# Performance work log

Measured on AMD Instinct MI355X. Metric: run time of the kernel, lower is better.

The kernel has to match this reference:

```python
import jax, jax.numpy as jnp
import numpy as np

BATCH, IN, HID, OUT = 8192, 784, 4096, 10


def setup_inputs() -> dict:
    key = jax.random.key(0)
    k_x, k_w1, k_b1, k_w2, k_b2 = jax.random.split(key, 5)
    return {
        "x": jax.random.normal(k_x, (BATCH, IN), dtype=jnp.float32),
        "W1": jax.random.normal(k_w1, (HID, IN), dtype=jnp.float32) * 0.05,
        "b1": jax.random.normal(k_b1, (HID,), dtype=jnp.float32) * 0.05,
        "W2": jax.random.normal(k_w2, (OUT, HID), dtype=jnp.float32) * 0.05,
        "b2": jax.random.normal(k_b2, (OUT,), dtype=jnp.float32) * 0.05,
    }


def reference(x, W1, b1, W2, b2):
    # x: [B, 784] -- first layer, so the input is NOT binarized (BNN convention
    # for in_features == 784); only the weight is sign-quantized.
    x = x.reshape(-1, IN)
    Wb1 = jnp.sign(W1)                       # binarized weights in {-1, 0, +1}
    h = jnp.einsum("bi,hi->bh", x, Wb1) + b1  # BinarizeLinear fc1
    h = jnp.clip(h, -1.0, 1.0)               # Hardtanh
    out = jnp.einsum("bh,oh->bo", h, W2) + b2  # plain float fc2
    return out
```

## Files before the change

kernel.cpp:

```cpp
#include <hip/hip_runtime.h>
#include <cstdint>


#define BATCH 8192
#define IN_F  784
#define HID   4096
#define OUT_F 10
#define KP    832
#define NKT   13
#define BM    256
#define BN    256
#define BK    64
#define NCT   (HID / BN)
#define HCS   264

typedef unsigned short u16;
typedef __attribute__((ext_vector_type(4))) unsigned short u16x4;
typedef __attribute__((ext_vector_type(8)))  _Float16 f16x8;
typedef __attribute__((ext_vector_type(4)))  float    f32x4;

#define BARRIER() do { asm volatile("" ::: "memory"); \
                       __builtin_amdgcn_s_barrier();  \
                       asm volatile("" ::: "memory"); } while (0)
#define WAITV(n)  asm volatile("s_waitcnt vmcnt(" #n ")" ::: "memory")
#define LGKM0()   asm volatile("s_waitcnt lgkmcnt(0)" ::: "memory")

__device__ __forceinline__ u16 f2h(float f) {
  union { _Float16 h; u16 u; } c;
  c.h = (_Float16)f;
  return c.u;
}

__device__ __forceinline__ void gl_lds16(const void* g, void* l) {
  __builtin_amdgcn_global_load_lds(
      (const __attribute__((address_space(1))) uint32_t*)g,
      (__attribute__((address_space(3))) uint32_t*)l, 16, 0, 0);
}

__global__ void prep_kernel(const float* __restrict__ x, const float* __restrict__ W1,
                            const float* __restrict__ W2,
                            u16* __restrict__ xh, u16* __restrict__ wh,
                            u16* __restrict__ w2h) {
  const int stride = gridDim.x * blockDim.x;
  const int gid = blockIdx.x * blockDim.x + threadIdx.x;
  const int KP4 = KP / 4;
  const int IN4 = IN_F / 4;
  const float4* x4 = (const float4*)x;
  const float4* w4 = (const float4*)W1;
  for (int i = gid; i < BATCH * KP4; i += stride) {
    int b = i / KP4, k = i - b * KP4;
    u16x4 o = {0, 0, 0, 0};
    if (k < IN4) {
      float4 v = x4[(size_t)b * IN4 + k];
      o[0] = f2h(v.x); o[1] = f2h(v.y); o[2] = f2h(v.z); o[3] = f2h(v.w);
    }
    *(u16x4*)&xh[(size_t)b * KP + k * 4] = o;
  }
  for (int i = gid; i < HID * KP4; i += stride) {
    int h = i / KP4, k = i - h * KP4;
    u16x4 o = {0, 0, 0, 0};
    if (k < IN4) {
      float4 v = w4[(size_t)h * IN4 + k];
      o[0] = v.x > 0.f ? 0x3C00 : (v.x < 0.f ? 0xBC00 : 0);
      o[1] = v.y > 0.f ? 0x3C00 : (v.y < 0.f ? 0xBC00 : 0);
      o[2] = v.z > 0.f ? 0x3C00 : (v.z < 0.f ? 0xBC00 : 0);
      o[3] = v.w > 0.f ? 0x3C00 : (v.w < 0.f ? 0xBC00 : 0);
    }
    *(u16x4*)&wh[(size_t)h * KP + k * 4] = o;
  }
  for (int i = gid; i < 16 * HID; i += stride) {
    int o = i >> 12, k = i & (HID - 1);
    w2h[i] = (o < OUT_F) ? f2h(W2[o * HID + k]) : (u16)0;
  }
}

__global__ void __launch_bounds__(512, 2) gemm_kernel(
    const u16* __restrict__ xh, const u16* __restrict__ wh,
    const u16* __restrict__ w2h, const float* __restrict__ b1,
    float* __restrict__ part) {
  __shared__ union {
    struct { u16 A[2][BM * BK]; u16 B[2][BN * BK]; } m;
    struct { u16 hc[128 * HCS]; u16 w2[16 * 256]; } e;
  } sm;

  const int t   = threadIdx.x;
  const int ct  = blockIdx.x;
  const int br  = blockIdx.y;
  const int w   = t >> 6;
  const int l   = t & 63;
  const int wm  = w >> 2;
  const int wn  = w & 3;
  const int g   = l >> 4;
  const int r16 = l & 15;
  const int swz = (r16 & 7) << 3;

  const int  srow  = t >> 3;
  const int  sslot = (t & 7) ^ (srow & 7);
  const u16* gA = xh + (size_t)(br * BM) * KP + sslot * 8;
  const u16* gB = wh + (size_t)(ct * BN) * KP + sslot * 8;

  auto stA2 = [&](int tile, int h) {
    const int b = tile & 1;
#pragma unroll
    for (int c = 2 * h; c < 2 * h + 2; ++c)
      gl_lds16(gA + (size_t)(c * 64 + srow) * KP + tile * BK,
               &sm.m.A[b][c * 4096 + t * 8]);
  };
  auto stB2 = [&](int tile, int h) {
    const int b = tile & 1;
#pragma unroll
    for (int c = 2 * h; c < 2 * h + 2; ++c)
      gl_lds16(gB + (size_t)(c * 64 + srow) * KP + tile * BK,
               &sm.m.B[b][c * 4096 + t * 8]);
  };
  auto rdA = [&](int p, int MI, int kk) -> f16x8 {
    int row = MI * 32 + wm * 16 + r16;
    return *(const f16x8*)&sm.m.A[p][row * 64 + ((kk * 32 + g * 8) ^ swz)];
  };
  auto rdB = [&](int p, int nj, int kk) -> f16x8 {
    int row = wn * 64 + nj * 16 + r16;
    return *(const f16x8*)&sm.m.B[p][row * 64 + ((kk * 32 + g * 8) ^ swz)];
  };

  f32x4 acc[8][4] = {};
  f16x8 af[4], bf0[4], bf1[4];

#define MFMA16(MH, BF) do {                                           \
    __builtin_amdgcn_s_setprio(1);                                    \
    _Pragma("unroll") for (int mi_ = 0; mi_ < 4; ++mi_)               \
      _Pragma("unroll") for (int nj_ = 0; nj_ < 4; ++nj_)             \
        acc[(MH) * 4 + mi_][nj_] = __builtin_amdgcn_mfma_f32_16x16x32_f16( \
            af[mi_], BF[nj_], acc[(MH) * 4 + mi_][nj_], 0, 0, 0);     \
    __builtin_amdgcn_s_setprio(0);                                    \
  } while (0)

  stA2(0, 0); stB2(0, 0); stB2(0, 1); stA2(0, 1);
  WAITV(2);
  BARRIER();

  for (int tt = 0; tt < NKT; ++tt) {
    const int  p    = tt & 1;
    const bool more = (tt + 1 < NKT);

#pragma unroll
    for (int mi = 0; mi < 4; ++mi) af[mi] = rdA(p, mi, 0);
#pragma unroll
    for (int nj = 0; nj < 4; ++nj) bf0[nj] = rdB(p, nj, 0);
    if (more) stA2(tt + 1, 0);
    BARRIER();
    MFMA16(0, bf0);
    if (more) { WAITV(2); } else { WAITV(0); }
    BARRIER();

#pragma unroll
    for (int mi = 0; mi < 4; ++mi) af[mi] = rdA(p, 4 + mi, 0);
    if (more) stB2(tt + 1, 0);
    BARRIER();
    MFMA16(1, bf0);
    BARRIER();

#pragma unroll
    for (int mi = 0; mi < 4; ++mi) af[mi] = rdA(p, mi, 1);
#pragma unroll
    for (int nj = 0; nj < 4; ++nj) bf1[nj] = rdB(p, nj, 1);
    if (more) stB2(tt + 1, 1);
    BARRIER();
    MFMA16(0, bf1);
    BARRIER();

#pragma unroll
    for (int mi = 0; mi < 4; ++mi) af[mi] = rdA(p, 4 + mi, 1);
    if (more) stA2(tt + 1, 1);
    BARRIER();
    MFMA16(1, bf1);
    if (more) WAITV(2);
    BARRIER();
  }

  LGKM0();
  BARRIER();
  {
    int row = t >> 5, sp = t & 31;
    int ls = (sp & 24) | ((sp ^ row) & 7);
    gl_lds16(w2h + (size_t)row * HID + ct * BN + ls * 8, &sm.e.w2[t * 8]);
  }
  float b1v[4];
#pragma unroll
  for (int ni = 0; ni < 4; ++ni) b1v[ni] = b1[ct * BN + wn * 64 + ni * 16 + r16];

  float* partBase = part + ((size_t)ct * BATCH + br * BM) * 16;

#pragma unroll
  for (int p = 0; p < 2; ++p) {
    if (p == 1) BARRIER();
#pragma unroll
    for (int mi = 0; mi < 4; ++mi)
#pragma unroll
      for (int ni = 0; ni < 4; ++ni)
#pragma unroll
        for (int r = 0; r < 4; ++r) {
          float v = acc[p * 4 + mi][ni][r] + b1v[ni];
          v = fminf(fmaxf(v, -1.f), 1.f);
          sm.e.hc[(mi * 32 + wm * 16 + g * 4 + r) * HCS + wn * 64 + ni * 16 + r16] = f2h(v);
        }
    if (p == 0) { WAITV(0); }
    BARRIER();
    f32x4 acc2 = {};
#pragma unroll
    for (int kk = 0; kk < 8; ++kk) {
      f16x8 a2 = *(const f16x8*)&sm.e.hc[(w * 16 + r16) * HCS + kk * 32 + g * 8];
      int s   = kk * 4 + g;
      int sp2 = (s & 24) | ((s ^ r16) & 7);
      f16x8 b2f = *(const f16x8*)&sm.e.w2[r16 * 256 + sp2 * 8];
      acc2 = __builtin_amdgcn_mfma_f32_16x16x32_f16(a2, b2f, acc2, 0, 0, 0);
    }
#pragma unroll
    for (int r = 0; r < 4; ++r)
      partBase[(size_t)(p * 128 + w * 16 + g * 4 + r) * 16 + r16] = acc2[r];
  }
}

__global__ void reduce_kernel(const float* __restrict__ part, const float* __restrict__ b2,
                              float* __restrict__ out) {
  int i = blockIdx.x * blockDim.x + threadIdx.x;
  if (i >= BATCH * OUT_F) return;
  int b = i / OUT_F, o = i - b * OUT_F;
  float acc = b2[o];
#pragma unroll
  for (int c = 0; c < NCT; ++c)
    acc += part[((size_t)c * BATCH + b) * 16 + o];
  out[i] = acc;
}

extern "C" void kernel_launch(void* const* d_in, const int* in_sizes, int n_in,
                              void* d_out, int out_size, void* d_ws, size_t ws_size,
                              hipStream_t stream) {
  const float* x  = (const float*)d_in[0];
  const float* W1 = (const float*)d_in[1];
  const float* b1 = (const float*)d_in[2];
  const float* W2 = (const float*)d_in[3];
  const float* b2 = (const float*)d_in[4];
  float* out = (float*)d_out;

  u16* xh  = (u16*)d_ws;
  u16* wh  = xh + (size_t)BATCH * KP;
  u16* w2h = wh + (size_t)HID * KP;
  float* part = (float*)(w2h + 16 * HID);

  hipLaunchKernelGGL(prep_kernel, dim3(2048), dim3(256), 0, stream, x, W1, W2, xh, wh, w2h);
  hipLaunchKernelGGL(gemm_kernel, dim3(NCT, BATCH / BM), dim3(512), 0, stream,
                     xh, wh, w2h, b1, part);
  hipLaunchKernelGGL(reduce_kernel, dim3((BATCH * OUT_F + 255) / 256), dim3(256), 0, stream,
                     part, b2, out);
}
```

Measured before the change: 65.77 us.

## Triple-buffer B tiles and prefetch them two K-steps ahead

Grows the weight-tile LDS staging from two to three buffers so B tiles are loaded two iterations ahead, while A stays double-buffered and both of its halves are issued earlier in the iteration. The goal is to hide more global-to-LDS load latency behind the MFMA work and to drop the mid-iteration vmcnt wait. The cost is extra LDS (now about 160KB per block) and a retuned wait-count schedule, which leaves little headroom and could stall if the counts are off.

```diff
diff --git a/kernel.cpp b/kernel.cpp
--- a/kernel.cpp
+++ b/kernel.cpp
@@ -79,7 +79,7 @@
     const u16* __restrict__ w2h, const float* __restrict__ b1,
     float* __restrict__ part) {
   __shared__ union {
-    struct { u16 A[2][BM * BK]; u16 B[2][BN * BK]; } m;
+    struct { u16 A[2][BM * BK]; u16 B[3][BN * BK]; } m;
     struct { u16 hc[128 * HCS]; u16 w2[16 * 256]; } e;
   } sm;
 
@@ -106,20 +106,19 @@
       gl_lds16(gA + (size_t)(c * 64 + srow) * KP + tile * BK,
                &sm.m.A[b][c * 4096 + t * 8]);
   };
-  auto stB2 = [&](int tile, int h) {
-    const int b = tile & 1;
+  auto stB2 = [&](int tile, int h, int s) {
 #pragma unroll
     for (int c = 2 * h; c < 2 * h + 2; ++c)
       gl_lds16(gB + (size_t)(c * 64 + srow) * KP + tile * BK,
-               &sm.m.B[b][c * 4096 + t * 8]);
+               &sm.m.B[s][c * 4096 + t * 8]);
   };
   auto rdA = [&](int p, int MI, int kk) -> f16x8 {
     int row = MI * 32 + wm * 16 + r16;
     return *(const f16x8*)&sm.m.A[p][row * 64 + ((kk * 32 + g * 8) ^ swz)];
   };
-  auto rdB = [&](int p, int nj, int kk) -> f16x8 {
+  auto rdB = [&](int s, int nj, int kk) -> f16x8 {
     int row = wn * 64 + nj * 16 + r16;
-    return *(const f16x8*)&sm.m.B[p][row * 64 + ((kk * 32 + g * 8) ^ swz)];
+    return *(const f16x8*)&sm.m.B[s][row * 64 + ((kk * 32 + g * 8) ^ swz)];
   };
 
   f32x4 acc[8][4] = {};
@@ -134,27 +133,31 @@
     __builtin_amdgcn_s_setprio(0);                                    \
   } while (0)
 
-  stA2(0, 0); stB2(0, 0); stB2(0, 1); stA2(0, 1);
-  WAITV(2);
+  stB2(0, 0, 0); stB2(0, 1, 0);
+  stA2(0, 0);    stA2(0, 1);
+  stB2(1, 0, 1); stB2(1, 1, 1);
+  WAITV(4);
   BARRIER();
 
   for (int tt = 0; tt < NKT; ++tt) {
-    const int  p    = tt & 1;
-    const bool more = (tt + 1 < NKT);
+    const int  p      = tt & 1;
+    const int  bs     = tt - (tt / 3) * 3;
+    const int  bs2    = (bs >= 1) ? bs - 1 : 2;
+    const bool a_more = (tt + 1 < NKT);
+    const bool b_more = (tt + 2 < NKT);
 
 #pragma unroll
     for (int mi = 0; mi < 4; ++mi) af[mi] = rdA(p, mi, 0);
 #pragma unroll
-    for (int nj = 0; nj < 4; ++nj) bf0[nj] = rdB(p, nj, 0);
-    if (more) stA2(tt + 1, 0);
+    for (int nj = 0; nj < 4; ++nj) bf0[nj] = rdB(bs, nj, 0);
+    if (a_more) stA2(tt + 1, 0);
     BARRIER();
     MFMA16(0, bf0);
-    if (more) { WAITV(2); } else { WAITV(0); }
     BARRIER();
 
 #pragma unroll
     for (int mi = 0; mi < 4; ++mi) af[mi] = rdA(p, 4 + mi, 0);
-    if (more) stB2(tt + 1, 0);
+    if (a_more) stA2(tt + 1, 1);
     BARRIER();
     MFMA16(1, bf0);
     BARRIER();
@@ -162,18 +165,19 @@
 #pragma unroll
     for (int mi = 0; mi < 4; ++mi) af[mi] = rdA(p, mi, 1);
 #pragma unroll
-    for (int nj = 0; nj < 4; ++nj) bf1[nj] = rdB(p, nj, 1);
-    if (more) stB2(tt + 1, 1);
+    for (int nj = 0; nj < 4; ++nj) bf1[nj] = rdB(bs, nj, 1);
+    if (b_more) stB2(tt + 2, 0, bs2);
     BARRIER();
     MFMA16(0, bf1);
     BARRIER();
 
 #pragma unroll
     for (int mi = 0; mi < 4; ++mi) af[mi] = rdA(p, 4 + mi, 1);
-    if (more) stA2(tt + 1, 1);
+    if (b_more) stB2(tt + 2, 1, bs2);
     BARRIER();
     MFMA16(1, bf1);
-    if (more) WAITV(2);
+    if      (tt < NKT - 2)  { WAITV(4); }
+    else if (tt == NKT - 2) { WAITV(0); }
     BARRIER();
   }
 
```

Measured after the change: 67.00 us. No clear change (+1.9%).

## Remap workgroups per XCD and merge epilogue into one swizzled pass

Applied to the files above, without the earlier changes.

The 2D grid becomes a 1D grid whose block index is remapped so that consecutive blocks on each XCD share the same pair of W1 column tiles, with the aim of improving L2 reuse of the weight operand. The fc2 epilogue now writes the whole clipped 256x256 hidden tile to LDS at once, using an XOR swizzle instead of row padding. It then runs the small MFMA in a single pass with two accumulators per wave, removing a barrier round and the two-phase loop. The larger LDS footprint and the launch bound lowered to one block per CU could reduce occupancy, though the previous main-loop buffers already limited it.

```diff
diff --git a/kernel.cpp b/kernel.cpp
--- a/kernel.cpp
+++ b/kernel.cpp
@@ -12,7 +12,6 @@
 #define BN    256
 #define BK    64
 #define NCT   (HID / BN)
-#define HCS   264
 
 typedef unsigned short u16;
 typedef __attribute__((ext_vector_type(4))) unsigned short u16x4;
@@ -74,18 +73,20 @@
   }
 }
 
-__global__ void __launch_bounds__(512, 2) gemm_kernel(
+__global__ void __launch_bounds__(512, 1) gemm_kernel(
     const u16* __restrict__ xh, const u16* __restrict__ wh,
     const u16* __restrict__ w2h, const float* __restrict__ b1,
     float* __restrict__ part) {
   __shared__ union {
     struct { u16 A[2][BM * BK]; u16 B[2][BN * BK]; } m;
-    struct { u16 hc[128 * HCS]; u16 w2[16 * 256]; } e;
+    struct { u16 hc[256 * 256]; u16 w2[16 * 256]; } e;
   } sm;
 
-  const int t   = threadIdx.x;
-  const int ct  = blockIdx.x;
-  const int br  = blockIdx.y;
+  const int t = threadIdx.x;
+  const int wg  = blockIdx.x;
+  const int swz_id = (wg & 7) * 64 + (wg >> 3);
+  const int ct  = swz_id >> 5;
+  const int br  = swz_id & 31;
   const int w   = t >> 6;
   const int l   = t & 63;
   const int wm  = w >> 2;
@@ -188,36 +189,41 @@
 #pragma unroll
   for (int ni = 0; ni < 4; ++ni) b1v[ni] = b1[ct * BN + wn * 64 + ni * 16 + r16];
 
+  auto hcAddr = [&](int row, int col) -> int {
+    return row * 256 + ((((col >> 3) ^ (row & 7)) << 3) | (col & 7));
+  };
+#pragma unroll
+  for (int MI = 0; MI < 8; ++MI)
+#pragma unroll
+    for (int ni = 0; ni < 4; ++ni)
+#pragma unroll
+      for (int r = 0; r < 4; ++r) {
+        float v = acc[MI][ni][r] + b1v[ni];
+        v = fminf(fmaxf(v, -1.f), 1.f);
+        sm.e.hc[hcAddr(MI * 32 + wm * 16 + g * 4 + r, wn * 64 + ni * 16 + r16)] = f2h(v);
+      }
+  LGKM0();
+  WAITV(0);
+  BARRIER();
+
   float* partBase = part + ((size_t)ct * BATCH + br * BM) * 16;
-
-#pragma unroll
-  for (int p = 0; p < 2; ++p) {
-    if (p == 1) BARRIER();
-#pragma unroll
-    for (int mi = 0; mi < 4; ++mi)
-#pragma unroll
-      for (int ni = 0; ni < 4; ++ni)
-#pragma unroll
-        for (int r = 0; r < 4; ++r) {
-          float v = acc[p * 4 + mi][ni][r] + b1v[ni];
-          v = fminf(fmaxf(v, -1.f), 1.f);
-          sm.e.hc[(mi * 32 + wm * 16 + g * 4 + r) * HCS + wn * 64 + ni * 16 + r16] = f2h(v);
-        }
-    if (p == 0) { WAITV(0); }
-    BARRIER();
-    f32x4 acc2 = {};
-#pragma unroll
-    for (int kk = 0; kk < 8; ++kk) {
-      f16x8 a2 = *(const f16x8*)&sm.e.hc[(w * 16 + r16) * HCS + kk * 32 + g * 8];
-      int s   = kk * 4 + g;
-      int sp2 = (s & 24) | ((s ^ r16) & 7);
-      f16x8 b2f = *(const f16x8*)&sm.e.w2[r16 * 256 + sp2 * 8];
-      acc2 = __builtin_amdgcn_mfma_f32_16x16x32_f16(a2, b2f, acc2, 0, 0, 0);
+  f32x4 acc2[2] = {};
+#pragma unroll
+  for (int kk = 0; kk < 8; ++kk) {
+    int s   = kk * 4 + g;
+    int sp2 = (s & 24) | ((s ^ r16) & 7);
+    f16x8 b2f = *(const f16x8*)&sm.e.w2[r16 * 256 + sp2 * 8];
+#pragma unroll
+    for (int mi = 0; mi < 2; ++mi) {
+      f16x8 a2 = *(const f16x8*)&sm.e.hc[hcAddr(w * 32 + mi * 16 + r16, kk * 32 + g * 8)];
+      acc2[mi] = __builtin_amdgcn_mfma_f32_16x16x32_f16(a2, b2f, acc2[mi], 0, 0, 0);
     }
+  }
+#pragma unroll
+  for (int mi = 0; mi < 2; ++mi)
 #pragma unroll
     for (int r = 0; r < 4; ++r)
-      partBase[(size_t)(p * 128 + w * 16 + g * 4 + r) * 16 + r16] = acc2[r];
-  }
+      partBase[(size_t)(w * 32 + mi * 16 + g * 4 + r) * 16 + r16] = acc2[mi][r];
 }
 
 __global__ void reduce_kernel(const float* __restrict__ part, const float* __restrict__ b2,
@@ -248,7 +254,7 @@
   float* part = (float*)(w2h + 16 * HID);
 
   hipLaunchKernelGGL(prep_kernel, dim3(2048), dim3(256), 0, stream, x, W1, W2, xh, wh, w2h);
-  hipLaunchKernelGGL(gemm_kernel, dim3(NCT, BATCH / BM), dim3(512), 0, stream,
+  hipLaunchKernelGGL(gemm_kernel, dim3(NCT * (BATCH / BM)), dim3(512), 0, stream,
                      xh, wh, w2h, b1, part);
   hipLaunchKernelGGL(reduce_kernel, dim3((BATCH * OUT_F + 255) / 256), dim3(256), 0, stream,
                      part, b2, out);
```

Result: slower. 67.98 us (+3.4%).
